# Optimization experiments

Hardware: AMD Instinct MI355X
Metric: run time of the kernel (lower is better)

Reference implementation:

```python
import jax, jax.numpy as jnp
import numpy as np

VOCAB0, VOCAB1 = 50257, 512
D_CONTENT, D_POS = 512, 512
D_EMB = D_CONTENT + D_POS
MAX_LEN = 4096
B = 32
T = 65536
EPS = 1e-3


def _seq_lens():
    lens = 1024 + np.arange(B, dtype=np.int64) * 66  # ragged lengths
    lens[-1] += T - lens.sum()                       # make them sum to T
    return lens


def setup_inputs() -> dict:
    key = jax.random.key(0)
    ks = jax.random.split(key, 6)
    lens = _seq_lens()
    # pos_ids = concat of arange(seq_len) per batch element (static, host-side)
    pos_ids = jnp.asarray(np.concatenate([np.arange(l) for l in lens]), dtype=jnp.int32)
    x0 = jax.random.randint(ks[0], (T,), 0, VOCAB0, dtype=jnp.int32)
    x1 = jax.random.randint(ks[1], (T,), 0, VOCAB1, dtype=jnp.int32)
    emb0_w = jax.random.normal(ks[2], (VOCAB0, D_CONTENT), dtype=jnp.float32) * 0.02
    emb1_w = jax.random.normal(ks[3], (VOCAB1, D_CONTENT), dtype=jnp.float32) * 0.02
    pos_table = jax.random.normal(ks[4], (MAX_LEN, D_POS), dtype=jnp.float32)
    a2 = jnp.ones((D_EMB,), dtype=jnp.float32)
    b2 = jnp.zeros((D_EMB,), dtype=jnp.float32)
    return {"x0": x0, "x1": x1, "pos_ids": pos_ids,
            "emb0_w": emb0_w, "emb1_w": emb1_w, "pos_table": pos_table,
            "a2": a2, "b2": b2}


def reference(x0, x1, pos_ids, emb0_w, emb1_w, pos_table, a2, b2):
    # summed embedding gathers (FeatureDropout is identity in eval mode)
    content = emb0_w[x0] + emb1_w[x1]                       # [T, D_CONTENT]
    # ragged position-table concat == gather by per-sequence position ids
    timing = pos_table[pos_ids]                              # [T, D_POS]
    z = jnp.concatenate([content, timing], axis=-1)          # [T, D_EMB] (partitioned)
    # LayerNormalization: torch.std is unbiased (ddof=1); divides by (sigma + eps)
    mu = jnp.mean(z, axis=-1, keepdims=True)
    zc = z - mu
    sigma = jnp.sqrt(jnp.sum(zc * zc, axis=-1, keepdims=True) / (z.shape[-1] - 1))
    annotations = zc / (sigma + EPS) * a2 + b2
    return annotations, timing
```

## Files before the change

kernel.cpp:

```cpp
#include <hip/hip_runtime.h>

#define DHALF  512
#define DEMB   1024
#define EPS    1e-3f

typedef float __attribute__((ext_vector_type(4))) f32x4;

__device__ __forceinline__ float4 f4add(float4 a, float4 b) {
    return make_float4(a.x + b.x, a.y + b.y, a.z + b.z, a.w + b.w);
}
__device__ __forceinline__ float f4sum(float4 a) { return a.x + a.y + a.z + a.w; }

__device__ __forceinline__ void nt_store4(float4 v, float4* p) {
    f32x4 t; t.x = v.x; t.y = v.y; t.z = v.z; t.w = v.w;
    __builtin_nontemporal_store(t, (f32x4*)p);
}

__global__ __launch_bounds__(256) void mle_kernel(
    const int* __restrict__ x0, const int* __restrict__ x1,
    const int* __restrict__ pos_ids,
    const float* __restrict__ emb0, const float* __restrict__ emb1,
    const float* __restrict__ post,
    const float* __restrict__ a2, const float* __restrict__ b2,
    float* __restrict__ ann, float* __restrict__ timing, int T)
{
    const int gtid = blockIdx.x * blockDim.x + threadIdx.x;
    const int tok  = gtid >> 6;
    const int lane = threadIdx.x & 63;
    if (tok >= T) return;

    const int i0 = x0[tok];
    const int i1 = x1[tok];
    const int ip = pos_ids[tok];

    const float4* r0 = (const float4*)(emb0 + (size_t)i0 * DHALF);
    const float4* r1 = (const float4*)(emb1 + (size_t)i1 * DHALF);
    const float4* rp = (const float4*)(post + (size_t)ip * DHALF);

    float4 cl = f4add(r0[lane],      r1[lane]);
    float4 ch = f4add(r0[lane + 64], r1[lane + 64]);
    float4 tl = rp[lane];
    float4 th = rp[lane + 64];

    float4* timv = (float4*)(timing + (size_t)tok * DHALF);
    nt_store4(tl, &timv[lane]);
    nt_store4(th, &timv[lane + 64]);

    const float4* A  = (const float4*)a2;
    const float4* Bv = (const float4*)b2;
    float4 acl = A[lane],        bcl = Bv[lane];
    float4 ach = A[lane + 64],   bch = Bv[lane + 64];
    float4 atl = A[lane + 128],  btl = Bv[lane + 128];
    float4 ath = A[lane + 192],  bth = Bv[lane + 192];

    float s = f4sum(cl) + f4sum(ch) + f4sum(tl) + f4sum(th);
    #pragma unroll
    for (int off = 32; off > 0; off >>= 1) s += __shfl_xor(s, off);
    const float mu = s * (1.0f / (float)DEMB);

    float4 zcl = make_float4(cl.x - mu, cl.y - mu, cl.z - mu, cl.w - mu);
    float4 zch = make_float4(ch.x - mu, ch.y - mu, ch.z - mu, ch.w - mu);
    float4 ztl = make_float4(tl.x - mu, tl.y - mu, tl.z - mu, tl.w - mu);
    float4 zth = make_float4(th.x - mu, th.y - mu, th.z - mu, th.w - mu);

    float q = zcl.x*zcl.x + zcl.y*zcl.y + zcl.z*zcl.z + zcl.w*zcl.w
            + zch.x*zch.x + zch.y*zch.y + zch.z*zch.z + zch.w*zch.w
            + ztl.x*ztl.x + ztl.y*ztl.y + ztl.z*ztl.z + ztl.w*ztl.w
            + zth.x*zth.x + zth.y*zth.y + zth.z*zth.z + zth.w*zth.w;
    #pragma unroll
    for (int off = 32; off > 0; off >>= 1) q += __shfl_xor(q, off);

    const float sigma = sqrtf(q * (1.0f / (float)(DEMB - 1)));
    const float inv   = 1.0f / (sigma + EPS);

    float4 ocl = make_float4(zcl.x*inv*acl.x + bcl.x, zcl.y*inv*acl.y + bcl.y,
                             zcl.z*inv*acl.z + bcl.z, zcl.w*inv*acl.w + bcl.w);
    float4 och = make_float4(zch.x*inv*ach.x + bch.x, zch.y*inv*ach.y + bch.y,
                             zch.z*inv*ach.z + bch.z, zch.w*inv*ach.w + bch.w);
    float4 otl = make_float4(ztl.x*inv*atl.x + btl.x, ztl.y*inv*atl.y + btl.y,
                             ztl.z*inv*atl.z + btl.z, ztl.w*inv*atl.w + btl.w);
    float4 oth = make_float4(zth.x*inv*ath.x + bth.x, zth.y*inv*ath.y + bth.y,
                             zth.z*inv*ath.z + bth.z, zth.w*inv*ath.w + bth.w);

    float4* annv = (float4*)(ann + (size_t)tok * DEMB);
    nt_store4(ocl, &annv[lane]);
    nt_store4(och, &annv[lane + 64]);
    nt_store4(otl, &annv[lane + 128]);
    nt_store4(oth, &annv[lane + 192]);
}

extern "C" void kernel_launch(void* const* d_in, const int* in_sizes, int n_in,
                              void* d_out, int out_size, void* d_ws, size_t ws_size,
                              hipStream_t stream) {
    const int*   x0     = (const int*)d_in[0];
    const int*   x1     = (const int*)d_in[1];
    const int*   pos    = (const int*)d_in[2];
    const float* emb0   = (const float*)d_in[3];
    const float* emb1   = (const float*)d_in[4];
    const float* ptab   = (const float*)d_in[5];
    const float* a2     = (const float*)d_in[6];
    const float* b2     = (const float*)d_in[7];

    const int T = in_sizes[0];
    float* out    = (float*)d_out;
    float* ann    = out;
    float* timing = out + (size_t)T * DEMB;

    const int threads = 256;
    const int blocks  = (T * 64 + threads - 1) / threads;
    mle_kernel<<<blocks, threads, 0, stream>>>(x0, x1, pos, emb0, emb1, ptab,
                                               a2, b2, ann, timing, T);
}
```

Before: 103.1 us.

## Process two tokens per wavefront with single-pass mean/variance reduction

Each wavefront now handles two tokens, which raises memory-level parallelism and reuses the a2/b2 loads across both tokens. The two separate reductions are merged into one: sum and sum of squares are reduced in a single shuffle loop, and variance is computed as E[x^2]-mu^2, clamped at zero. This halves the dependent shuffle chains and the grid size, and adds occupancy hints to launch bounds. In exchange it uses more registers per thread, and the one-pass variance can lose precision. There is no guard for tokB when T is odd.

```diff
diff --git a/kernel.cpp b/kernel.cpp
--- a/kernel.cpp
+++ b/kernel.cpp
@@ -10,13 +10,22 @@
     return make_float4(a.x + b.x, a.y + b.y, a.z + b.z, a.w + b.w);
 }
 __device__ __forceinline__ float f4sum(float4 a) { return a.x + a.y + a.z + a.w; }
+__device__ __forceinline__ float f4sq(float4 a)  { return a.x*a.x + a.y*a.y + a.z*a.z + a.w*a.w; }
 
 __device__ __forceinline__ void nt_store4(float4 v, float4* p) {
     f32x4 t; t.x = v.x; t.y = v.y; t.z = v.z; t.w = v.w;
     __builtin_nontemporal_store(t, (f32x4*)p);
 }
 
-__global__ __launch_bounds__(256) void mle_kernel(
+__device__ __forceinline__ float4 norm4(float4 v, float mu, float inv,
+                                        float4 av, float4 bv) {
+    return make_float4((v.x - mu) * inv * av.x + bv.x,
+                       (v.y - mu) * inv * av.y + bv.y,
+                       (v.z - mu) * inv * av.z + bv.z,
+                       (v.w - mu) * inv * av.w + bv.w);
+}
+
+__global__ __launch_bounds__(256, 4) void mle_kernel(
     const int* __restrict__ x0, const int* __restrict__ x1,
     const int* __restrict__ pos_ids,
     const float* __restrict__ emb0, const float* __restrict__ emb1,
@@ -24,69 +33,74 @@
     const float* __restrict__ a2, const float* __restrict__ b2,
     float* __restrict__ ann, float* __restrict__ timing, int T)
 {
-    const int gtid = blockIdx.x * blockDim.x + threadIdx.x;
-    const int tok  = gtid >> 6;
+    const int wid  = threadIdx.x >> 6;
     const int lane = threadIdx.x & 63;
-    if (tok >= T) return;
+    const int tokA = (blockIdx.x * 4 + wid) * 2;
+    const int tokB = tokA + 1;
+    if (tokA >= T) return;
 
-    const int i0 = x0[tok];
-    const int i1 = x1[tok];
-    const int ip = pos_ids[tok];
+    const int i0A = x0[tokA], i1A = x1[tokA], ipA = pos_ids[tokA];
+    const int i0B = x0[tokB], i1B = x1[tokB], ipB = pos_ids[tokB];
 
-    const float4* r0 = (const float4*)(emb0 + (size_t)i0 * DHALF);
-    const float4* r1 = (const float4*)(emb1 + (size_t)i1 * DHALF);
-    const float4* rp = (const float4*)(post + (size_t)ip * DHALF);
+    const float4* r0A = (const float4*)(emb0 + (size_t)i0A * DHALF);
+    const float4* r1A = (const float4*)(emb1 + (size_t)i1A * DHALF);
+    const float4* rpA = (const float4*)(post + (size_t)ipA * DHALF);
+    const float4* r0B = (const float4*)(emb0 + (size_t)i0B * DHALF);
+    const float4* r1B = (const float4*)(emb1 + (size_t)i1B * DHALF);
+    const float4* rpB = (const float4*)(post + (size_t)ipB * DHALF);
 
-    float4 cl = f4add(r0[lane],      r1[lane]);
-    float4 ch = f4add(r0[lane + 64], r1[lane + 64]);
-    float4 tl = rp[lane];
-    float4 th = rp[lane + 64];
+    float4 clA = f4add(r0A[lane],      r1A[lane]);
+    float4 chA = f4add(r0A[lane + 64], r1A[lane + 64]);
+    float4 tlA = rpA[lane];
+    float4 thA = rpA[lane + 64];
+    float4 clB = f4add(r0B[lane],      r1B[lane]);
+    float4 chB = f4add(r0B[lane + 64], r1B[lane + 64]);
+    float4 tlB = rpB[lane];
+    float4 thB = rpB[lane + 64];
 
-    float4* timv = (float4*)(timing + (size_t)tok * DHALF);
-    nt_store4(tl, &timv[lane]);
-    nt_store4(th, &timv[lane + 64]);
+    float4* timvA = (float4*)(timing + (size_t)tokA * DHALF);
+    float4* timvB = (float4*)(timing + (size_t)tokB * DHALF);
+    nt_store4(tlA, &timvA[lane]);
+    nt_store4(thA, &timvA[lane + 64]);
+    nt_store4(tlB, &timvB[lane]);
+    nt_store4(thB, &timvB[lane + 64]);
 
-    const float4* A  = (const float4*)a2;
+    const float4* Av = (const float4*)a2;
     const float4* Bv = (const float4*)b2;
-    float4 acl = A[lane],        bcl = Bv[lane];
-    float4 ach = A[lane + 64],   bch = Bv[lane + 64];
-    float4 atl = A[lane + 128],  btl = Bv[lane + 128];
-    float4 ath = A[lane + 192],  bth = Bv[lane + 192];
+    float4 acl = Av[lane],        bcl = Bv[lane];
+    float4 ach = Av[lane + 64],   bch = Bv[lane + 64];
+    float4 atl = Av[lane + 128],  btl = Bv[lane + 128];
+    float4 ath = Av[lane + 192],  bth = Bv[lane + 192];
 
-    float s = f4sum(cl) + f4sum(ch) + f4sum(tl) + f4sum(th);
+    float sA = f4sum(clA) + f4sum(chA) + f4sum(tlA) + f4sum(thA);
+    float qA = f4sq(clA)  + f4sq(chA)  + f4sq(tlA)  + f4sq(thA);
+    float sB = f4sum(clB) + f4sum(chB) + f4sum(tlB) + f4sum(thB);
+    float qB = f4sq(clB)  + f4sq(chB)  + f4sq(tlB)  + f4sq(thB);
     #pragma unroll
-    for (int off = 32; off > 0; off >>= 1) s += __shfl_xor(s, off);
-    const float mu = s * (1.0f / (float)DEMB);
+    for (int off = 32; off > 0; off >>= 1) {
+        sA += __shfl_xor(sA, off);
+        qA += __shfl_xor(qA, off);
+        sB += __shfl_xor(sB, off);
+        qB += __shfl_xor(qB, off);
+    }
+    const float muA = sA * (1.0f / (float)DEMB);
+    const float muB = sB * (1.0f / (float)DEMB);
+    const float varA = fmaxf(qA - sA * muA, 0.0f) * (1.0f / (float)(DEMB - 1));
+    const float varB = fmaxf(qB - sB * muB, 0.0f) * (1.0f / (float)(DEMB - 1));
+    const float invA = 1.0f / (sqrtf(varA) + EPS);
+    const float invB = 1.0f / (sqrtf(varB) + EPS);
 
-    float4 zcl = make_float4(cl.x - mu, cl.y - mu, cl.z - mu, cl.w - mu);
-    float4 zch = make_float4(ch.x - mu, ch.y - mu, ch.z - mu, ch.w - mu);
-    float4 ztl = make_float4(tl.x - mu, tl.y - mu, tl.z - mu, tl.w - mu);
-    float4 zth = make_float4(th.x - mu, th.y - mu, th.z - mu, th.w - mu);
+    float4* annvA = (float4*)(ann + (size_t)tokA * DEMB);
+    float4* annvB = (float4*)(ann + (size_t)tokB * DEMB);
 
-    float q = zcl.x*zcl.x + zcl.y*zcl.y + zcl.z*zcl.z + zcl.w*zcl.w
-            + zch.x*zch.x + zch.y*zch.y + zch.z*zch.z + zch.w*zch.w
-            + ztl.x*ztl.x + ztl.y*ztl.y + ztl.z*ztl.z + ztl.w*ztl.w
-            + zth.x*zth.x + zth.y*zth.y + zth.z*zth.z + zth.w*zth.w;
-    #pragma unroll
-    for (int off = 32; off > 0; off >>= 1) q += __shfl_xor(q, off);
-
-    const float sigma = sqrtf(q * (1.0f / (float)(DEMB - 1)));
-    const float inv   = 1.0f / (sigma + EPS);
-
-    float4 ocl = make_float4(zcl.x*inv*acl.x + bcl.x, zcl.y*inv*acl.y + bcl.y,
-                             zcl.z*inv*acl.z + bcl.z, zcl.w*inv*acl.w + bcl.w);
-    float4 och = make_float4(zch.x*inv*ach.x + bch.x, zch.y*inv*ach.y + bch.y,
-                             zch.z*inv*ach.z + bch.z, zch.w*inv*ach.w + bch.w);
-    float4 otl = make_float4(ztl.x*inv*atl.x + btl.x, ztl.y*inv*atl.y + btl.y,
-                             ztl.z*inv*atl.z + btl.z, ztl.w*inv*atl.w + btl.w);
-    float4 oth = make_float4(zth.x*inv*ath.x + bth.x, zth.y*inv*ath.y + bth.y,
-                             zth.z*inv*ath.z + bth.z, zth.w*inv*ath.w + bth.w);
-
-    float4* annv = (float4*)(ann + (size_t)tok * DEMB);
-    nt_store4(ocl, &annv[lane]);
-    nt_store4(och, &annv[lane + 64]);
-    nt_store4(otl, &annv[lane + 128]);
-    nt_store4(oth, &annv[lane + 192]);
+    nt_store4(norm4(clA, muA, invA, acl, bcl), &annvA[lane]);
+    nt_store4(norm4(chA, muA, invA, ach, bch), &annvA[lane + 64]);
+    nt_store4(norm4(tlA, muA, invA, atl, btl), &annvA[lane + 128]);
+    nt_store4(norm4(thA, muA, invA, ath, bth), &annvA[lane + 192]);
+    nt_store4(norm4(clB, muB, invB, acl, bcl), &annvB[lane]);
+    nt_store4(norm4(chB, muB, invB, ach, bch), &annvB[lane + 64]);
+    nt_store4(norm4(tlB, muB, invB, atl, btl), &annvB[lane + 128]);
+    nt_store4(norm4(thB, muB, invB, ath, bth), &annvB[lane + 192]);
 }
 
 extern "C" void kernel_launch(void* const* d_in, const int* in_sizes, int n_in,
@@ -107,7 +121,7 @@
     float* timing = out + (size_t)T * DEMB;
 
     const int threads = 256;
-    const int blocks  = (T * 64 + threads - 1) / threads;
+    const int blocks  = (T + 7) / 8;
     mle_kernel<<<blocks, threads, 0, stream>>>(x0, x1, pos, emb0, emb1, ptab,
                                                a2, b2, ann, timing, T);
 }
```

Result: no change. 103.2 us (+0.1%).
